# Performance work log

Hardware: AMD Instinct MI355X
Metric: run time of the kernel (lower is better)

## Reference

```python
import jax, jax.numpy as jnp
import numpy as np

N_U, N_I, E, H = 100000, 50000, 1000000, 128


def setup_inputs() -> dict:
    key = jax.random.key(0)
    ks = jax.random.split(key, 12)
    s = 1.0 / np.sqrt(H)
    return {
        "x_user": jax.random.normal(ks[0], (N_U, H), jnp.float32),
        "x_item": jax.random.normal(ks[1], (N_I, H), jnp.float32),
        "W0": jax.random.normal(ks[2], (H, H), jnp.float32) * s,
        "b0": jnp.zeros((H,), jnp.float32),
        "W1": jax.random.normal(ks[3], (H, H), jnp.float32) * s,
        "b1": jnp.zeros((H,), jnp.float32),
        "W2": jax.random.normal(ks[4], (2 * H, H), jnp.float32) * s,
        "b2": jnp.zeros((H,), jnp.float32),
        "W3": jax.random.normal(ks[5], (2 * H, H), jnp.float32) * s,
        "b3": jnp.zeros((H,), jnp.float32),
        "Wp": jax.random.normal(ks[6], (2 * H, 2), jnp.float32) * s,
        "bp": jnp.zeros((2,), jnp.float32),
        "edge_src": jax.random.randint(ks[7], (E,), 0, N_U, jnp.int32),
        "edge_dst": jax.random.randint(ks[8], (E,), 0, N_I, jnp.int32),
    }


def _inv_sqrt_deg(idx, n):
    # DGL GraphConv: degrees clamped to min 1 before norm
    deg = jax.ops.segment_sum(jnp.ones_like(idx, jnp.float32), idx, num_segments=n)
    return jax.lax.rsqrt(jnp.maximum(deg, 1.0))


def reference(x_user, x_item, W0, b0, W1, b1, W2, b2, W3, b3, Wp, bp,
              edge_src, edge_dst):
    ones_e = None  # degrees computed from edge lists
    inv_du = _inv_sqrt_deg(edge_src, N_U)  # user degree in 'evaluate' edges
    inv_di = _inv_sqrt_deg(edge_dst, N_I)  # item degree in 'evaluate' edges

    # relation 'evaluate' (user -> item), GraphConv(h0, h0), norm='both'
    m_u = x_user * inv_du[:, None]
    agg_item = jax.ops.segment_sum(m_u[edge_src], edge_dst, num_segments=N_I)
    h_item = (agg_item * inv_di[:, None]) @ W0 + b0

    # relation 'evaluated' (item -> user, reversed edges), GraphConv(h1, h1)
    m_i = x_item * inv_di[:, None]
    agg_user = jax.ops.segment_sum(m_i[edge_dst], edge_src, num_segments=N_U)
    h_user = (agg_user * inv_du[:, None]) @ W1 + b1

    h_user = jax.nn.relu(h_user)
    h_item = jax.nn.relu(h_item)

    # concat with inputs, then per-type linear (conv2 / conv3)
    t_user = jnp.concatenate([x_user, h_user], axis=1) @ W2 + b2
    t_item = jnp.concatenate([x_item, h_item], axis=1) @ W3 + b3

    # MLPPredictor over user->item edges: gather-cat-linear
    feat_e = jnp.concatenate([t_user[edge_src], t_item[edge_dst]], axis=1)
    score = feat_e @ Wp + bp
    return jax.nn.softmax(score, axis=1)
```

## Files before the change

### kernel.cpp

```cpp
#include <hip/hip_runtime.h>
#include <hip/hip_bf16.h>


#define H 128
#define CAPU 1536
#define CAPI 3072

typedef __attribute__((ext_vector_type(8))) short bf16x8;
typedef __attribute__((ext_vector_type(4))) float f32x4;

__device__ __forceinline__ unsigned short f2bf(float f) {
    unsigned u = __float_as_uint(f);
    unsigned r = (u + 0x7fffu + ((u >> 16) & 1u)) >> 16;
    return (unsigned short)r;
}
__device__ __forceinline__ float bflo(unsigned b) { return __uint_as_float(b << 16); }
__device__ __forceinline__ float bfhi(unsigned b) { return __uint_as_float(b & 0xffff0000u); }
__device__ __forceinline__ float bfu(unsigned short b) { return __uint_as_float((unsigned)b << 16); }

__global__ __launch_bounds__(256) void p1_partition(
    const int* __restrict__ src, const int* __restrict__ dst,
    int* __restrict__ gCurU, int* __restrict__ gCurI,
    unsigned* __restrict__ pairU, unsigned* __restrict__ pairI,
    int E, int nbu, int nbi) {
    __shared__ int cntU[1024], baseU[1024], cntI[512], baseI[512];
    int t0 = blockIdx.x * 2048;
    for (int i = threadIdx.x; i < nbu; i += 256) cntU[i] = 0;
    for (int i = threadIdx.x; i < nbi; i += 256) cntI[i] = 0;
    __syncthreads();
    #pragma unroll
    for (int j = 0; j < 8; ++j) {
        int e = t0 + j * 256 + threadIdx.x;
        if (e < E) { atomicAdd(&cntU[src[e] >> 7], 1); atomicAdd(&cntI[dst[e] >> 7], 1); }
    }
    __syncthreads();
    for (int i = threadIdx.x; i < nbu; i += 256) {
        int c = cntU[i];
        baseU[i] = c ? (CAPU * i + atomicAdd(&gCurU[i], c)) : 0;
    }
    for (int i = threadIdx.x; i < nbi; i += 256) {
        int c = cntI[i];
        baseI[i] = c ? (CAPI * i + atomicAdd(&gCurI[i], c)) : 0;
    }
    __syncthreads();
    #pragma unroll
    for (int j = 0; j < 8; ++j) {
        int e = t0 + j * 256 + threadIdx.x;
        if (e < E) {
            int s = src[e], d = dst[e];
            int bu = s >> 7, bi = d >> 7;
            int r1 = atomicSub(&cntU[bu], 1) - 1;
            int idx1 = baseU[bu] + r1;
            if (idx1 < CAPU * (bu + 1))
                pairU[idx1] = ((unsigned)(s & 127) << 24) | (unsigned)d;
            int r2 = atomicSub(&cntI[bi], 1) - 1;
            int idx2 = baseI[bi] + r2;
            if (idx2 < CAPI * (bi + 1))
                pairI[idx2] = ((unsigned)(d & 127) << 24) | (unsigned)s;
        }
    }
}

__global__ __launch_bounds__(256) void p2_build(
    const unsigned* __restrict__ pairU, const unsigned* __restrict__ pairI,
    const int* __restrict__ gCurU, const int* __restrict__ gCurI,
    int2* __restrict__ offU, int2* __restrict__ offI,
    float* __restrict__ invU, float* __restrict__ invI,
    int* __restrict__ valU, int* __restrict__ valI,
    int NU, int NI, int NBU, int shiftU, int shiftI) {
    __shared__ int cnt[1024], pref[1024], part[256];
    __shared__ int out[CAPI];
    bool us = blockIdx.x < (unsigned)NBU;
    int b = us ? blockIdx.x : blockIdx.x - NBU;
    const unsigned* pairs = us ? pairU : pairI;
    int cap = us ? CAPU : CAPI;
    int size = us ? gCurU[b] : gCurI[b];
    if (size > cap) size = cap;
    int start = b * cap;
    int shift = us ? shiftU : shiftI;
    int2* off = us ? offU : offI;
    float* inv = us ? invU : invI;
    int* val = us ? valU : valI;
    int n = us ? NU : NI;
    int t = threadIdx.x;

    for (int i = t; i < 1024; i += 256) cnt[i] = 0;
    __syncthreads();
    for (int i = t; i < size; i += 256) {
        unsigned p = pairs[start + i];
        int key = (int)((p >> 24) << 3) | (int)((p & 0xFFFFFFu) >> shift);
        atomicAdd(&cnt[key], 1);
    }
    __syncthreads();
    int b4 = t * 4;
    int s0 = cnt[b4], s1 = cnt[b4 + 1], s2 = cnt[b4 + 2], s3 = cnt[b4 + 3];
    int tot = s0 + s1 + s2 + s3;
    part[t] = tot; __syncthreads();
    for (int o2 = 1; o2 < 256; o2 <<= 1) {
        int v = (t >= o2) ? part[t - o2] : 0; __syncthreads();
        part[t] += v; __syncthreads();
    }
    int excl = part[t] - tot;
    pref[b4] = excl;
    pref[b4 + 1] = excl + s0;
    pref[b4 + 2] = excl + s0 + s1;
    pref[b4 + 3] = excl + s0 + s1 + s2;
    __syncthreads();
    if (t < 128) {
        int node = (b << 7) + t;
        if (node < n) {
            int st = pref[t * 8];
            int en = (t == 127) ? size : pref[t * 8 + 8];
            off[node] = make_int2(start + st, start + en);
            inv[node] = rsqrtf(fmaxf((float)(en - st), 1.0f));
        }
    }
    __syncthreads();
    for (int i = t; i < size; i += 256) {
        unsigned p = pairs[start + i];
        int key = (int)((p >> 24) << 3) | (int)((p & 0xFFFFFFu) >> shift);
        int r = atomicAdd(&pref[key], 1);
        out[r] = (int)(p & 0xFFFFFFu);
    }
    __syncthreads();
    for (int i = t; i < size; i += 256) val[start + i] = out[i];
}

__global__ void prep_kernel(const float* __restrict__ W0, const float* __restrict__ W1,
                            const float* __restrict__ W2, const float* __restrict__ b2,
                            const float* __restrict__ W3, const float* __restrict__ b3,
                            const float* __restrict__ Wp, const float* __restrict__ bp,
                            float* __restrict__ mats,
                            unsigned short* __restrict__ WswU, unsigned short* __restrict__ WswI) {
    if (blockIdx.x == 0) {
        int tid = threadIdx.x;
        int j = tid >> 1, c = tid & 1;
        float ax = 0.f, ah = 0.f, bx = 0.f, bh = 0.f;
        for (int m = 0; m < H; ++m) {
            float wpu = Wp[m * 2 + c];
            float wpi = Wp[(H + m) * 2 + c];
            ax += W2[j * H + m] * wpu;
            ah += W2[(H + j) * H + m] * wpu;
            bx += W3[j * H + m] * wpi;
            bh += W3[(H + j) * H + m] * wpi;
        }
        mats[      j * 2 + c] = ax;
        mats[256 + j * 2 + c] = ah;
        mats[512 + j * 2 + c] = bx;
        mats[768 + j * 2 + c] = bh;
        if (tid < 2) {
            float s1 = 0.f, s2 = 0.f;
            for (int m = 0; m < H; ++m) {
                s1 += b2[m] * Wp[m * 2 + tid];
                s2 += b3[m] * Wp[(H + m) * 2 + tid];
            }
            mats[1024 + tid] = s1 + bp[tid];
            mats[1026 + tid] = s2;
        }
    } else {
        const float* W = (blockIdx.x == 1) ? W0 : W1;
        unsigned short* o = (blockIdx.x == 1) ? WswU : WswI;
        for (int i = threadIdx.x; i < 4096; i += 256) {
            float4 w = ((const float4*)W)[i];
            int k = i >> 5, n0 = (i & 31) * 4;
            int kb = k >> 3, kj = k & 7;
            o[(kb * 128 + n0 + 0) * 8 + kj] = f2bf(w.x);
            o[(kb * 128 + n0 + 1) * 8 + kj] = f2bf(w.y);
            o[(kb * 128 + n0 + 2) * 8 + kj] = f2bf(w.z);
            o[(kb * 128 + n0 + 3) * 8 + kj] = f2bf(w.w);
        }
    }
}

__global__ __launch_bounds__(256) void mfma_node(
    const float* __restrict__ xU, const float* __restrict__ xI,
    const float* __restrict__ invU, const float* __restrict__ invI,
    const unsigned short* __restrict__ WswU, const unsigned short* __restrict__ WswI,
    unsigned short* __restrict__ yU, unsigned short* __restrict__ yI,
    const float* __restrict__ mats,
    float2* __restrict__ gxU, float2* __restrict__ gxI,
    int NU, int NI, int TU) {
    __shared__ __align__(16) unsigned short SM[32768];
    unsigned short* Ws = SM;
    unsigned short* As = SM + 16384;

    bool us = blockIdx.x < (unsigned)TU;
    int tile = us ? blockIdx.x : blockIdx.x - TU;
    const float* x = us ? xU : xI;
    const float* inv = us ? invU : invI;
    const unsigned short* Wsw = us ? WswU : WswI;
    unsigned short* y = us ? yU : yI;
    const float* Mx = mats + (us ? 0 : 512);
    const float* cv = mats + (us ? 1024 : 1026);
    float2* gx = us ? gxU : gxI;
    int n = us ? NU : NI;
    int row0 = tile << 7;

    for (int i = threadIdx.x; i < 2048; i += 256)
        ((float4*)Ws)[i] = ((const float4*)Wsw)[i];
    for (int it = 0; it < 16; ++it) {
        int i = it * 256 + threadIdx.x;
        int m = i >> 5, c4 = i & 31;
        int row = row0 + m;
        float4 v = (row < n) ? ((const float4*)x)[(size_t)row * 32 + c4]
                             : make_float4(0.f, 0.f, 0.f, 0.f);
        int k0 = c4 * 4;
        ushort4 s4; s4.x = f2bf(v.x); s4.y = f2bf(v.y); s4.z = f2bf(v.z); s4.w = f2bf(v.w);
        *(ushort4*)&As[((k0 >> 3) * 128 + m) * 8 + (k0 & 7)] = s4;
    }
    __syncthreads();

    int w = threadIdx.x >> 6, l = threadIdx.x & 63;
    int lane15 = l & 15, quad = l >> 4;

    f32x4 acc[2][8];
    #pragma unroll
    for (int rt = 0; rt < 2; ++rt)
        #pragma unroll
        for (int c = 0; c < 8; ++c) acc[rt][c] = (f32x4){0.f, 0.f, 0.f, 0.f};

    #pragma unroll
    for (int ks = 0; ks < 4; ++ks) {
        int kb = ks * 4 + quad;
        bf16x8 a0 = *(const bf16x8*)&As[(kb * 128 + w * 32 + lane15) * 8];
        bf16x8 a1 = *(const bf16x8*)&As[(kb * 128 + w * 32 + 16 + lane15) * 8];
        #pragma unroll
        for (int c = 0; c < 8; ++c) {
            bf16x8 b = *(const bf16x8*)&Ws[(kb * 128 + c * 16 + lane15) * 8];
            acc[0][c] = __builtin_amdgcn_mfma_f32_16x16x32_bf16(a0, b, acc[0][c], 0, 0, 0);
            acc[1][c] = __builtin_amdgcn_mfma_f32_16x16x32_bf16(a1, b, acc[1][c], 0, 0, 0);
        }
    }

    {
        int row = threadIdx.x >> 1, cc = threadIdx.x & 1;
        float p = 0.f;
        for (int kb = 0; kb < 16; ++kb) {
            const unsigned short* ap = &As[(kb * 128 + row) * 8];
            #pragma unroll
            for (int j = 0; j < 8; ++j)
                p += bfu(ap[j]) * Mx[(kb * 8 + j) * 2 + cc];
        }
        int grow = row0 + row;
        if (grow < n) ((float*)&gx[grow])[cc] = p + cv[cc];
    }
    __syncthreads();

    const int LSTR = 136;
    unsigned short* Lw = SM + w * 32 * LSTR;
    #pragma unroll
    for (int rt = 0; rt < 2; ++rt) {
        #pragma unroll
        for (int r = 0; r < 4; ++r) {
            int lrow = rt * 16 + quad * 4 + r;
            int grow = row0 + w * 32 + lrow;
            float iv = (grow < n) ? inv[grow] : 0.f;
            #pragma unroll
            for (int c = 0; c < 8; ++c)
                Lw[lrow * LSTR + c * 16 + lane15] = f2bf(acc[rt][c][r] * iv);
        }
    }
    #pragma unroll
    for (int pass = 0; pass < 8; ++pass) {
        int lrow = pass * 4 + quad;
        int grow = row0 + w * 32 + lrow;
        uint4 v = *(uint4*)&Lw[lrow * LSTR + lane15 * 8];
        if (grow < n) *(uint4*)&y[(size_t)grow * 128 + lane15 * 8] = v;
    }
}

__global__ __launch_bounds__(256) void gather_kernel(
    const int2* __restrict__ offU, const int* __restrict__ valU,
    const int2* __restrict__ offI, const int* __restrict__ valI,
    const unsigned short* __restrict__ yU, const unsigned short* __restrict__ yI,
    const float* __restrict__ invU, const float* __restrict__ invI,
    const float* __restrict__ b0, const float* __restrict__ b1,
    const float* __restrict__ mats,
    const float2* __restrict__ gxU, const float2* __restrict__ gxI,
    float2* __restrict__ su, float2* __restrict__ si,
    int NU, int NI, int GU) {
    bool us = blockIdx.x < (unsigned)GU;
    int nb = us ? blockIdx.x : blockIdx.x - GU;
    const int2* off = us ? offU : offI;
    const int* val = us ? valU : valI;
    const unsigned short* yo = us ? yI : yU;
    const float* inv = us ? invU : invI;
    const float* bv = us ? b1 : b0;
    const float* Mh = mats + (us ? 256 : 768);
    const float2* gx = us ? gxU : gxI;
    float2* so = us ? su : si;
    int n = us ? NU : NI;

    int g = threadIdx.x >> 4, t = threadIdx.x & 15, j0 = t * 8;
    int u = nb * 16 + g;
    if (u >= n) return;

    float a0 = 0, a1 = 0, a2 = 0, a3 = 0, a4 = 0, a5 = 0, a6 = 0, a7 = 0;
    int2 oe = off[u];
    int k = oe.x, end = oe.y;
    for (; k + 4 <= end; k += 4) {
        int v0 = val[k], v1 = val[k + 1], v2 = val[k + 2], v3 = val[k + 3];
        uint4 w0 = *(const uint4*)(yo + (size_t)v0 * H + j0);
        uint4 w1 = *(const uint4*)(yo + (size_t)v1 * H + j0);
        uint4 w2 = *(const uint4*)(yo + (size_t)v2 * H + j0);
        uint4 w3 = *(const uint4*)(yo + (size_t)v3 * H + j0);
        a0 += bflo(w0.x) + bflo(w1.x) + bflo(w2.x) + bflo(w3.x);
        a1 += bfhi(w0.x) + bfhi(w1.x) + bfhi(w2.x) + bfhi(w3.x);
        a2 += bflo(w0.y) + bflo(w1.y) + bflo(w2.y) + bflo(w3.y);
        a3 += bfhi(w0.y) + bfhi(w1.y) + bfhi(w2.y) + bfhi(w3.y);
        a4 += bflo(w0.z) + bflo(w1.z) + bflo(w2.z) + bflo(w3.z);
        a5 += bfhi(w0.z) + bfhi(w1.z) + bfhi(w2.z) + bfhi(w3.z);
        a6 += bflo(w0.w) + bflo(w1.w) + bflo(w2.w) + bflo(w3.w);
        a7 += bfhi(w0.w) + bfhi(w1.w) + bfhi(w2.w) + bfhi(w3.w);
    }
    for (; k < end; ++k) {
        int v0 = val[k];
        uint4 w0 = *(const uint4*)(yo + (size_t)v0 * H + j0);
        a0 += bflo(w0.x); a1 += bfhi(w0.x); a2 += bflo(w0.y); a3 += bfhi(w0.y);
        a4 += bflo(w0.z); a5 += bfhi(w0.z); a6 += bflo(w0.w); a7 += bfhi(w0.w);
    }
    float iv = inv[u];
    float4 bb0 = *(const float4*)(bv + j0), bb1 = *(const float4*)(bv + j0 + 4);
    float h0 = fmaxf(a0 * iv + bb0.x, 0.f), h1 = fmaxf(a1 * iv + bb0.y, 0.f);
    float h2 = fmaxf(a2 * iv + bb0.z, 0.f), h3 = fmaxf(a3 * iv + bb0.w, 0.f);
    float h4 = fmaxf(a4 * iv + bb1.x, 0.f), h5 = fmaxf(a5 * iv + bb1.y, 0.f);
    float h6 = fmaxf(a6 * iv + bb1.z, 0.f), h7 = fmaxf(a7 * iv + bb1.w, 0.f);
    float4 m0 = *(const float4*)(Mh + j0 * 2),      m1 = *(const float4*)(Mh + j0 * 2 + 4);
    float4 m2 = *(const float4*)(Mh + j0 * 2 + 8),  m3 = *(const float4*)(Mh + j0 * 2 + 12);
    float p0 = h0 * m0.x + h1 * m0.z + h2 * m1.x + h3 * m1.z
             + h4 * m2.x + h5 * m2.z + h6 * m3.x + h7 * m3.z;
    float p1 = h0 * m0.y + h1 * m0.w + h2 * m1.y + h3 * m1.w
             + h4 * m2.y + h5 * m2.w + h6 * m3.y + h7 * m3.w;
    #pragma unroll
    for (int o = 1; o < 16; o <<= 1) { p0 += __shfl_xor(p0, o); p1 += __shfl_xor(p1, o); }
    if (t == 0) {
        float2 gg = gx[u];
        so[u] = make_float2(p0 + gg.x, p1 + gg.y);
    }
}

__global__ void edge_kernel(const int* __restrict__ src, const int* __restrict__ dst,
                            const float2* __restrict__ su, const float2* __restrict__ si,
                            float2* __restrict__ out, int E) {
    int e0 = (blockIdx.x * 256 + threadIdx.x) * 2;
    if (e0 >= E) return;
    int2 s2 = *(const int2*)(src + e0);
    int2 d2 = *(const int2*)(dst + e0);
    float2 a = su[s2.x], b = si[d2.x];
    float l0 = a.x + b.x, l1 = a.y + b.y;
    float m = fmaxf(l0, l1);
    float q0 = __expf(l0 - m), q1 = __expf(l1 - m);
    float r = 1.0f / (q0 + q1);
    out[e0] = make_float2(q0 * r, q1 * r);
    if (e0 + 1 < E) {
        a = su[s2.y]; b = si[d2.y];
        l0 = a.x + b.x; l1 = a.y + b.y;
        m = fmaxf(l0, l1);
        q0 = __expf(l0 - m); q1 = __expf(l1 - m);
        r = 1.0f / (q0 + q1);
        out[e0 + 1] = make_float2(q0 * r, q1 * r);
    }
}

extern "C" void kernel_launch(void* const* d_in, const int* in_sizes, int n_in,
                              void* d_out, int out_size, void* d_ws, size_t ws_size,
                              hipStream_t stream) {
    const float* x_user = (const float*)d_in[0];
    const float* x_item = (const float*)d_in[1];
    const float* W0 = (const float*)d_in[2];
    const float* b0 = (const float*)d_in[3];
    const float* W1 = (const float*)d_in[4];
    const float* b1 = (const float*)d_in[5];
    const float* W2 = (const float*)d_in[6];
    const float* b2 = (const float*)d_in[7];
    const float* W3 = (const float*)d_in[8];
    const float* b3 = (const float*)d_in[9];
    const float* Wp = (const float*)d_in[10];
    const float* bp = (const float*)d_in[11];
    const int* esrc = (const int*)d_in[12];
    const int* edst = (const int*)d_in[13];

    const int NU = in_sizes[0] / H;
    const int NI = in_sizes[1] / H;
    const int E  = in_sizes[12];
    const int NBU = (NU + 127) >> 7;
    const int NBI = (NI + 127) >> 7;
    const int GU = (NU + 15) >> 4, GI = (NI + 15) >> 4;
    auto topshift = [](int n) {
        int bits = 32 - __builtin_clz((unsigned)(n - 1));
        return bits > 3 ? bits - 3 : 0;
    };
    const int shiftU = topshift(NI);
    const int shiftI = topshift(NU);

    auto rnd = [](size_t x) { return (x + 63) & ~(size_t)63; };
    char* base = (char*)d_ws;
    size_t o = 0;
    auto alloc = [&](size_t elems) { void* p = base + o * 4; o += rnd(elems); return p; };

    float* inv_du = (float*)alloc(NU);
    float* inv_di = (float*)alloc(NI);
    float2* su    = (float2*)alloc((size_t)NU * 2);
    float2* si    = (float2*)alloc((size_t)NI * 2);
    float2* gxU   = (float2*)alloc((size_t)NU * 2);
    float2* gxI   = (float2*)alloc((size_t)NI * 2);
    float* mats   = (float*)alloc(1056);
    size_t cur_off = o;
    int* gCurU = (int*)alloc(NBU);
    int* gCurI = (int*)alloc(NBI);
    size_t cur_words = o - cur_off;
    int2* offU = (int2*)alloc((size_t)NU * 2);
    int2* offI = (int2*)alloc((size_t)NI * 2);
    int* valU  = (int*)alloc((size_t)NBU * CAPU);
    int* valI  = (int*)alloc((size_t)NBI * CAPI);
    unsigned* pairU = (unsigned*)alloc((size_t)NBU * CAPU);
    unsigned* pairI = (unsigned*)alloc((size_t)NBI * CAPI);
    unsigned short* WswU = (unsigned short*)alloc(8192);
    unsigned short* WswI = (unsigned short*)alloc(8192);
    unsigned short* yU = (unsigned short*)alloc((size_t)NU * 64);
    unsigned short* yI = (unsigned short*)alloc((size_t)NI * 64);

    hipMemsetAsync(gCurU, 0, cur_words * 4, stream);

    prep_kernel<<<3, 256, 0, stream>>>(W0, W1, W2, b2, W3, b3, Wp, bp, mats, WswU, WswI);

    p1_partition<<<(E + 2047) / 2048, 256, 0, stream>>>(
        esrc, edst, gCurU, gCurI, pairU, pairI, E, NBU, NBI);
    p2_build<<<NBU + NBI, 256, 0, stream>>>(
        pairU, pairI, gCurU, gCurI, offU, offI, inv_du, inv_di, valU, valI,
        NU, NI, NBU, shiftU, shiftI);

    mfma_node<<<NBU + NBI, 256, 0, stream>>>(
        x_user, x_item, inv_du, inv_di, WswU, WswI, yU, yI, mats, gxU, gxI, NU, NI, NBU);

    gather_kernel<<<GU + GI, 256, 0, stream>>>(
        offU, valU, offI, valI, yU, yI, inv_du, inv_di, b0, b1, mats,
        gxU, gxI, su, si, NU, NI, GU);

    edge_kernel<<<(E / 2 + 255) / 256, 256, 0, stream>>>(esrc, edst, su, si, (float2*)d_out, E);
}
```

Measured before the change: 310.3 us.

## Merge prep with partition and CSR build with MFMA node transform

Folds the weight prep kernel into the edge partition launch, and runs the CSR build and MFMA node-transform blocks in one launch. Because the MFMA transform now runs concurrently with the degree computation, it no longer scales by the source inverse degree. The gather kernel instead multiplies each neighbour row by its own inverse degree. The MFMA path also reads B fragments straight from global memory rather than staging W in shared memory. This cuts kernel launches and lets the two independent stages overlap, at the cost of an extra per-edge inverse-degree load in the gather and uncached weight reads in the MFMA loop.

```diff
diff --git a/kernel.cpp b/kernel.cpp
--- a/kernel.cpp
+++ b/kernel.cpp
@@ -18,13 +18,61 @@
 __device__ __forceinline__ float bfhi(unsigned b) { return __uint_as_float(b & 0xffff0000u); }
 __device__ __forceinline__ float bfu(unsigned short b) { return __uint_as_float((unsigned)b << 16); }
 
-__global__ __launch_bounds__(256) void p1_partition(
+__global__ __launch_bounds__(256) void k1_prep_p1(
+    const float* __restrict__ W0, const float* __restrict__ W1,
+    const float* __restrict__ W2, const float* __restrict__ b2,
+    const float* __restrict__ W3, const float* __restrict__ b3,
+    const float* __restrict__ Wp, const float* __restrict__ bp,
+    float* __restrict__ mats,
+    unsigned short* __restrict__ WswU, unsigned short* __restrict__ WswI,
     const int* __restrict__ src, const int* __restrict__ dst,
     int* __restrict__ gCurU, int* __restrict__ gCurI,
     unsigned* __restrict__ pairU, unsigned* __restrict__ pairI,
     int E, int nbu, int nbi) {
     __shared__ int cntU[1024], baseU[1024], cntI[512], baseI[512];
-    int t0 = blockIdx.x * 2048;
+    int bx = blockIdx.x;
+    if (bx == 0) {
+        int tid = threadIdx.x;
+        int j = tid >> 1, c = tid & 1;
+        float ax = 0.f, ah = 0.f, bx2 = 0.f, bh = 0.f;
+        for (int m = 0; m < H; ++m) {
+            float wpu = Wp[m * 2 + c];
+            float wpi = Wp[(H + m) * 2 + c];
+            ax += W2[j * H + m] * wpu;
+            ah += W2[(H + j) * H + m] * wpu;
+            bx2 += W3[j * H + m] * wpi;
+            bh += W3[(H + j) * H + m] * wpi;
+        }
+        mats[      j * 2 + c] = ax;
+        mats[256 + j * 2 + c] = ah;
+        mats[512 + j * 2 + c] = bx2;
+        mats[768 + j * 2 + c] = bh;
+        if (tid < 2) {
+            float s1 = 0.f, s2 = 0.f;
+            for (int m = 0; m < H; ++m) {
+                s1 += b2[m] * Wp[m * 2 + tid];
+                s2 += b3[m] * Wp[(H + m) * 2 + tid];
+            }
+            mats[1024 + tid] = s1 + bp[tid];
+            mats[1026 + tid] = s2;
+        }
+        return;
+    }
+    if (bx <= 2) {
+        const float* W = (bx == 1) ? W0 : W1;
+        unsigned short* o = (bx == 1) ? WswU : WswI;
+        for (int i = threadIdx.x; i < 4096; i += 256) {
+            float4 w = ((const float4*)W)[i];
+            int k = i >> 5, n0 = (i & 31) * 4;
+            int kb = k >> 3, kj = k & 7;
+            o[(kb * 128 + n0 + 0) * 8 + kj] = f2bf(w.x);
+            o[(kb * 128 + n0 + 1) * 8 + kj] = f2bf(w.y);
+            o[(kb * 128 + n0 + 2) * 8 + kj] = f2bf(w.z);
+            o[(kb * 128 + n0 + 3) * 8 + kj] = f2bf(w.w);
+        }
+        return;
+    }
+    int t0 = (bx - 3) * 2048;
     for (int i = threadIdx.x; i < nbu; i += 256) cntU[i] = 0;
     for (int i = threadIdx.x; i < nbi; i += 256) cntI[i] = 0;
     __syncthreads();
@@ -61,133 +109,88 @@
     }
 }
 
-__global__ __launch_bounds__(256) void p2_build(
+__global__ __launch_bounds__(256) void k2_build_mfma(
     const unsigned* __restrict__ pairU, const unsigned* __restrict__ pairI,
     const int* __restrict__ gCurU, const int* __restrict__ gCurI,
     int2* __restrict__ offU, int2* __restrict__ offI,
     float* __restrict__ invU, float* __restrict__ invI,
     int* __restrict__ valU, int* __restrict__ valI,
-    int NU, int NI, int NBU, int shiftU, int shiftI) {
-    __shared__ int cnt[1024], pref[1024], part[256];
-    __shared__ int out[CAPI];
-    bool us = blockIdx.x < (unsigned)NBU;
-    int b = us ? blockIdx.x : blockIdx.x - NBU;
-    const unsigned* pairs = us ? pairU : pairI;
-    int cap = us ? CAPU : CAPI;
-    int size = us ? gCurU[b] : gCurI[b];
-    if (size > cap) size = cap;
-    int start = b * cap;
-    int shift = us ? shiftU : shiftI;
-    int2* off = us ? offU : offI;
-    float* inv = us ? invU : invI;
-    int* val = us ? valU : valI;
-    int n = us ? NU : NI;
-    int t = threadIdx.x;
-
-    for (int i = t; i < 1024; i += 256) cnt[i] = 0;
-    __syncthreads();
-    for (int i = t; i < size; i += 256) {
-        unsigned p = pairs[start + i];
-        int key = (int)((p >> 24) << 3) | (int)((p & 0xFFFFFFu) >> shift);
-        atomicAdd(&cnt[key], 1);
-    }
-    __syncthreads();
-    int b4 = t * 4;
-    int s0 = cnt[b4], s1 = cnt[b4 + 1], s2 = cnt[b4 + 2], s3 = cnt[b4 + 3];
-    int tot = s0 + s1 + s2 + s3;
-    part[t] = tot; __syncthreads();
-    for (int o2 = 1; o2 < 256; o2 <<= 1) {
-        int v = (t >= o2) ? part[t - o2] : 0; __syncthreads();
-        part[t] += v; __syncthreads();
-    }
-    int excl = part[t] - tot;
-    pref[b4] = excl;
-    pref[b4 + 1] = excl + s0;
-    pref[b4 + 2] = excl + s0 + s1;
-    pref[b4 + 3] = excl + s0 + s1 + s2;
-    __syncthreads();
-    if (t < 128) {
-        int node = (b << 7) + t;
-        if (node < n) {
-            int st = pref[t * 8];
-            int en = (t == 127) ? size : pref[t * 8 + 8];
-            off[node] = make_int2(start + st, start + en);
-            inv[node] = rsqrtf(fmaxf((float)(en - st), 1.0f));
-        }
-    }
-    __syncthreads();
-    for (int i = t; i < size; i += 256) {
-        unsigned p = pairs[start + i];
-        int key = (int)((p >> 24) << 3) | (int)((p & 0xFFFFFFu) >> shift);
-        int r = atomicAdd(&pref[key], 1);
-        out[r] = (int)(p & 0xFFFFFFu);
-    }
-    __syncthreads();
-    for (int i = t; i < size; i += 256) val[start + i] = out[i];
-}
-
-__global__ void prep_kernel(const float* __restrict__ W0, const float* __restrict__ W1,
-                            const float* __restrict__ W2, const float* __restrict__ b2,
-                            const float* __restrict__ W3, const float* __restrict__ b3,
-                            const float* __restrict__ Wp, const float* __restrict__ bp,
-                            float* __restrict__ mats,
-                            unsigned short* __restrict__ WswU, unsigned short* __restrict__ WswI) {
-    if (blockIdx.x == 0) {
-        int tid = threadIdx.x;
-        int j = tid >> 1, c = tid & 1;
-        float ax = 0.f, ah = 0.f, bx = 0.f, bh = 0.f;
-        for (int m = 0; m < H; ++m) {
-            float wpu = Wp[m * 2 + c];
-            float wpi = Wp[(H + m) * 2 + c];
-            ax += W2[j * H + m] * wpu;
-            ah += W2[(H + j) * H + m] * wpu;
-            bx += W3[j * H + m] * wpi;
-            bh += W3[(H + j) * H + m] * wpi;
-        }
-        mats[      j * 2 + c] = ax;
-        mats[256 + j * 2 + c] = ah;
-        mats[512 + j * 2 + c] = bx;
-        mats[768 + j * 2 + c] = bh;
-        if (tid < 2) {
-            float s1 = 0.f, s2 = 0.f;
-            for (int m = 0; m < H; ++m) {
-                s1 += b2[m] * Wp[m * 2 + tid];
-                s2 += b3[m] * Wp[(H + m) * 2 + tid];
-            }
-            mats[1024 + tid] = s1 + bp[tid];
-            mats[1026 + tid] = s2;
-        }
-    } else {
-        const float* W = (blockIdx.x == 1) ? W0 : W1;
-        unsigned short* o = (blockIdx.x == 1) ? WswU : WswI;
-        for (int i = threadIdx.x; i < 4096; i += 256) {
-            float4 w = ((const float4*)W)[i];
-            int k = i >> 5, n0 = (i & 31) * 4;
-            int kb = k >> 3, kj = k & 7;
-            o[(kb * 128 + n0 + 0) * 8 + kj] = f2bf(w.x);
-            o[(kb * 128 + n0 + 1) * 8 + kj] = f2bf(w.y);
-            o[(kb * 128 + n0 + 2) * 8 + kj] = f2bf(w.z);
-            o[(kb * 128 + n0 + 3) * 8 + kj] = f2bf(w.w);
-        }
-    }
-}
-
-__global__ __launch_bounds__(256) void mfma_node(
     const float* __restrict__ xU, const float* __restrict__ xI,
-    const float* __restrict__ invU, const float* __restrict__ invI,
     const unsigned short* __restrict__ WswU, const unsigned short* __restrict__ WswI,
     unsigned short* __restrict__ yU, unsigned short* __restrict__ yI,
     const float* __restrict__ mats,
     float2* __restrict__ gxU, float2* __restrict__ gxI,
-    int NU, int NI, int TU) {
-    __shared__ __align__(16) unsigned short SM[32768];
-    unsigned short* Ws = SM;
-    unsigned short* As = SM + 16384;
-
-    bool us = blockIdx.x < (unsigned)TU;
-    int tile = us ? blockIdx.x : blockIdx.x - TU;
+    int NU, int NI, int NBU, int NBI, int shiftU, int shiftI) {
+    __shared__ __align__(16) char SMEM[34816];
+    int nP2 = NBU + NBI;
+    int t = threadIdx.x;
+
+    if (blockIdx.x < (unsigned)nP2) {
+        int* cnt  = (int*)SMEM;
+        int* pref = cnt + 1024;
+        int* part = pref + 1024;
+        int* out  = part + 256;
+        bool us = blockIdx.x < (unsigned)NBU;
+        int b = us ? blockIdx.x : blockIdx.x - NBU;
+        const unsigned* pairs = us ? pairU : pairI;
+        int cap = us ? CAPU : CAPI;
+        int size = us ? gCurU[b] : gCurI[b];
+        if (size > cap) size = cap;
+        int start = b * cap;
+        int shift = us ? shiftU : shiftI;
+        int2* off = us ? offU : offI;
+        float* inv = us ? invU : invI;
+        int* val = us ? valU : valI;
+        int n = us ? NU : NI;
+
+        for (int i = t; i < 1024; i += 256) cnt[i] = 0;
+        __syncthreads();
+        for (int i = t; i < size; i += 256) {
+            unsigned p = pairs[start + i];
+            int key = (int)((p >> 24) << 3) | (int)((p & 0xFFFFFFu) >> shift);
+            atomicAdd(&cnt[key], 1);
+        }
+        __syncthreads();
+        int b4 = t * 4;
+        int s0 = cnt[b4], s1 = cnt[b4 + 1], s2 = cnt[b4 + 2], s3 = cnt[b4 + 3];
+        int tot = s0 + s1 + s2 + s3;
+        part[t] = tot; __syncthreads();
+        for (int o2 = 1; o2 < 256; o2 <<= 1) {
+            int v = (t >= o2) ? part[t - o2] : 0; __syncthreads();
+            part[t] += v; __syncthreads();
+        }
+        int excl = part[t] - tot;
+        pref[b4] = excl;
+        pref[b4 + 1] = excl + s0;
+        pref[b4 + 2] = excl + s0 + s1;
+        pref[b4 + 3] = excl + s0 + s1 + s2;
+        __syncthreads();
+        if (t < 128) {
+            int node = (b << 7) + t;
+            if (node < n) {
+                int st = pref[t * 8];
+                int en = (t == 127) ? size : pref[t * 8 + 8];
+                off[node] = make_int2(start + st, start + en);
+                inv[node] = rsqrtf(fmaxf((float)(en - st), 1.0f));
+            }
+        }
+        __syncthreads();
+        for (int i = t; i < size; i += 256) {
+            unsigned p = pairs[start + i];
+            int key = (int)((p >> 24) << 3) | (int)((p & 0xFFFFFFu) >> shift);
+            int r = atomicAdd(&pref[key], 1);
+            out[r] = (int)(p & 0xFFFFFFu);
+        }
+        __syncthreads();
+        for (int i = t; i < size; i += 256) val[start + i] = out[i];
+        return;
+    }
+
+    unsigned short* As = (unsigned short*)SMEM;
+    int mb = blockIdx.x - nP2;
+    bool us = mb < NBU;
+    int tile = us ? mb : mb - NBU;
     const float* x = us ? xU : xI;
-    const float* inv = us ? invU : invI;
     const unsigned short* Wsw = us ? WswU : WswI;
     unsigned short* y = us ? yU : yI;
     const float* Mx = mats + (us ? 0 : 512);
@@ -196,10 +199,8 @@
     int n = us ? NU : NI;
     int row0 = tile << 7;
 
-    for (int i = threadIdx.x; i < 2048; i += 256)
-        ((float4*)Ws)[i] = ((const float4*)Wsw)[i];
     for (int it = 0; it < 16; ++it) {
-        int i = it * 256 + threadIdx.x;
+        int i = it * 256 + t;
         int m = i >> 5, c4 = i & 31;
         int row = row0 + m;
         float4 v = (row < n) ? ((const float4*)x)[(size_t)row * 32 + c4]
@@ -210,7 +211,7 @@
     }
     __syncthreads();
 
-    int w = threadIdx.x >> 6, l = threadIdx.x & 63;
+    int w = t >> 6, l = t & 63;
     int lane15 = l & 15, quad = l >> 4;
 
     f32x4 acc[2][8];
@@ -226,14 +227,14 @@
         bf16x8 a1 = *(const bf16x8*)&As[(kb * 128 + w * 32 + 16 + lane15) * 8];
         #pragma unroll
         for (int c = 0; c < 8; ++c) {
-            bf16x8 b = *(const bf16x8*)&Ws[(kb * 128 + c * 16 + lane15) * 8];
+            bf16x8 b = *(const bf16x8*)&Wsw[(size_t)(kb * 128 + c * 16 + lane15) * 8];
             acc[0][c] = __builtin_amdgcn_mfma_f32_16x16x32_bf16(a0, b, acc[0][c], 0, 0, 0);
             acc[1][c] = __builtin_amdgcn_mfma_f32_16x16x32_bf16(a1, b, acc[1][c], 0, 0, 0);
         }
     }
 
     {
-        int row = threadIdx.x >> 1, cc = threadIdx.x & 1;
+        int row = t >> 1, cc = t & 1;
         float p = 0.f;
         for (int kb = 0; kb < 16; ++kb) {
             const unsigned short* ap = &As[(kb * 128 + row) * 8];
@@ -247,17 +248,16 @@
     __syncthreads();
 
     const int LSTR = 136;
-    unsigned short* Lw = SM + w * 32 * LSTR;
+    unsigned short* SMu = (unsigned short*)SMEM;
+    unsigned short* Lw = SMu + w * 32 * LSTR;
     #pragma unroll
     for (int rt = 0; rt < 2; ++rt) {
         #pragma unroll
         for (int r = 0; r < 4; ++r) {
             int lrow = rt * 16 + quad * 4 + r;
-            int grow = row0 + w * 32 + lrow;
-            float iv = (grow < n) ? inv[grow] : 0.f;
             #pragma unroll
             for (int c = 0; c < 8; ++c)
-                Lw[lrow * LSTR + c * 16 + lane15] = f2bf(acc[rt][c][r] * iv);
+                Lw[lrow * LSTR + c * 16 + lane15] = f2bf(acc[rt][c][r]);
         }
     }
     #pragma unroll
@@ -284,6 +284,7 @@
     const int2* off = us ? offU : offI;
     const int* val = us ? valU : valI;
     const unsigned short* yo = us ? yI : yU;
+    const float* invo = us ? invI : invU;
     const float* inv = us ? invU : invI;
     const float* bv = us ? b1 : b0;
     const float* Mh = mats + (us ? 256 : 768);
@@ -300,24 +301,28 @@
     int k = oe.x, end = oe.y;
     for (; k + 4 <= end; k += 4) {
         int v0 = val[k], v1 = val[k + 1], v2 = val[k + 2], v3 = val[k + 3];
+        float i0 = invo[v0], i1 = invo[v1], i2 = invo[v2], i3 = invo[v3];
         uint4 w0 = *(const uint4*)(yo + (size_t)v0 * H + j0);
         uint4 w1 = *(const uint4*)(yo + (size_t)v1 * H + j0);
         uint4 w2 = *(const uint4*)(yo + (size_t)v2 * H + j0);
         uint4 w3 = *(const uint4*)(yo + (size_t)v3 * H + j0);
-        a0 += bflo(w0.x) + bflo(w1.x) + bflo(w2.x) + bflo(w3.x);
-        a1 += bfhi(w0.x) + bfhi(w1.x) + bfhi(w2.x) + bfhi(w3.x);
-        a2 += bflo(w0.y) + bflo(w1.y) + bflo(w2.y) + bflo(w3.y);
-        a3 += bfhi(w0.y) + bfhi(w1.y) + bfhi(w2.y) + bfhi(w3.y);
-        a4 += bflo(w0.z) + bflo(w1.z) + bflo(w2.z) + bflo(w3.z);
-        a5 += bfhi(w0.z) + bfhi(w1.z) + bfhi(w2.z) + bfhi(w3.z);
-        a6 += bflo(w0.w) + bflo(w1.w) + bflo(w2.w) + bflo(w3.w);
-        a7 += bfhi(w0.w) + bfhi(w1.w) + bfhi(w2.w) + bfhi(w3.w);
+        a0 += bflo(w0.x) * i0 + bflo(w1.x) * i1 + bflo(w2.x) * i2 + bflo(w3.x) * i3;
+        a1 += bfhi(w0.x) * i0 + bfhi(w1.x) * i1 + bfhi(w2.x) * i2 + bfhi(w3.x) * i3;
+        a2 += bflo(w0.y) * i0 + bflo(w1.y) * i1 + bflo(w2.y) * i2 + bflo(w3.y) * i3;
+        a3 += bfhi(w0.y) * i0 + bfhi(w1.y) * i1 + bfhi(w2.y) * i2 + bfhi(w3.y) * i3;
+        a4 += bflo(w0.z) * i0 + bflo(w1.z) * i1 + bflo(w2.z) * i2 + bflo(w3.z) * i3;
+        a5 += bfhi(w0.z) * i0 + bfhi(w1.z) * i1 + bfhi(w2.z) * i2 + bfhi(w3.z) * i3;
+        a6 += bflo(w0.w) * i0 + bflo(w1.w) * i1 + bflo(w2.w) * i2 + bflo(w3.w) * i3;
+        a7 += bfhi(w0.w) * i0 + bfhi(w1.w) * i1 + bfhi(w2.w) * i2 + bfhi(w3.w) * i3;
     }
     for (; k < end; ++k) {
         int v0 = val[k];
+        float i0 = invo[v0];
         uint4 w0 = *(const uint4*)(yo + (size_t)v0 * H + j0);
-        a0 += bflo(w0.x); a1 += bfhi(w0.x); a2 += bflo(w0.y); a3 += bfhi(w0.y);
-        a4 += bflo(w0.z); a5 += bfhi(w0.z); a6 += bflo(w0.w); a7 += bfhi(w0.w);
+        a0 += bflo(w0.x) * i0; a1 += bfhi(w0.x) * i0;
+        a2 += bflo(w0.y) * i0; a3 += bfhi(w0.y) * i0;
+        a4 += bflo(w0.z) * i0; a5 += bfhi(w0.z) * i0;
+        a6 += bflo(w0.w) * i0; a7 += bfhi(w0.w) * i0;
     }
     float iv = inv[u];
     float4 bb0 = *(const float4*)(bv + j0), bb1 = *(const float4*)(bv + j0 + 4);
@@ -422,16 +427,15 @@
 
     hipMemsetAsync(gCurU, 0, cur_words * 4, stream);
 
-    prep_kernel<<<3, 256, 0, stream>>>(W0, W1, W2, b2, W3, b3, Wp, bp, mats, WswU, WswI);
-
-    p1_partition<<<(E + 2047) / 2048, 256, 0, stream>>>(
+    int p1_blocks = (E + 2047) / 2048;
+    k1_prep_p1<<<3 + p1_blocks, 256, 0, stream>>>(
+        W0, W1, W2, b2, W3, b3, Wp, bp, mats, WswU, WswI,
         esrc, edst, gCurU, gCurI, pairU, pairI, E, NBU, NBI);
-    p2_build<<<NBU + NBI, 256, 0, stream>>>(
+
+    k2_build_mfma<<<2 * (NBU + NBI), 256, 0, stream>>>(
         pairU, pairI, gCurU, gCurI, offU, offI, inv_du, inv_di, valU, valI,
-        NU, NI, NBU, shiftU, shiftI);
-
-    mfma_node<<<NBU + NBI, 256, 0, stream>>>(
-        x_user, x_item, inv_du, inv_di, WswU, WswI, yU, yI, mats, gxU, gxI, NU, NI, NBU);
+        x_user, x_item, WswU, WswI, yU, yI, mats, gxU, gxI,
+        NU, NI, NBU, NBI, shiftU, shiftI);
 
     gather_kernel<<<GU + GI, 256, 0, stream>>>(
         offU, valU, offI, valI, yU, yI, inv_du, inv_di, b0, b1, mats,
```

Result: faster. 303.1 us (-2.3%).
